# Kernel tuning notes

Measured on AMD Instinct MI355X. Metric: run time of the kernel, lower is better.

The kernel has to match this reference:

```python
import jax, jax.numpy as jnp
import numpy as np

D_HID = 512
N_HEADS = 16
D_HEAD = D_HID // N_HEADS  # 32
D_FFN = 2048
B, N = 4, 1024
FACTOR = 0.5 / np.sqrt(D_HEAD)
EPS = 1e-5


def layer_norm(x, g, b):
    m = x.mean(-1, keepdims=True)
    v = ((x - m) ** 2).mean(-1, keepdims=True)
    return (x - m) / jnp.sqrt(v + EPS) * g + b


def setup_inputs() -> dict:
    key = jax.random.key(0)
    ks = jax.random.split(key, 24)
    s = 0.02
    p = lambda k, shape: jax.random.normal(k, shape, jnp.float32) * s
    inp = {
        'H': jax.random.normal(ks[0], (B, N, D_HID), jnp.float32),
        'V': jax.random.normal(ks[1], (B, N, 3, D_HID), jnp.float32),
        'D_batch': jax.random.normal(ks[2], (B, N, N), jnp.float32),
        'rbf_bias': jax.random.normal(ks[3], (B, 1, N, N), jnp.float32),
        'H_mask': jax.random.randint(ks[4], (B, N), 0, 2, jnp.int32),
        # attention sublayer params
        'g1': jnp.ones((D_HID,), jnp.float32), 'beta1': jnp.zeros((D_HID,), jnp.float32),
        'Wq': p(ks[5], (D_HID, 4 * D_HID)), 'bq': p(ks[6], (4 * D_HID,)),
        'Wk': p(ks[7], (D_HID, 4 * D_HID)), 'bk': p(ks[8], (4 * D_HID,)),
        'Wv': p(ks[9], (D_HID, D_HID)), 'bv': p(ks[10], (D_HID,)),
        'Wvv': p(ks[11], (D_HID, D_HID)),
        'Wo': p(ks[12], (D_HID, D_HID)), 'bo': p(ks[13], (D_HID,)),
        'Wvo': p(ks[14], (D_HID, D_HID)),
        # GVP FFN sublayer params
        'g2': jnp.ones((D_HID,), jnp.float32), 'beta2': jnp.zeros((D_HID,), jnp.float32),
        'Wlv': p(ks[15], (D_HID, 2 * D_HID)),
        'W1': p(ks[16], (2 * D_HID, D_FFN)), 'b1f': p(ks[17], (D_FFN,)),
        'W2': p(ks[18], (D_FFN, 2 * D_HID)), 'b2f': p(ks[19], (2 * D_HID,)),
    }
    return inp


def ept_forward(H, V, D_batch, rbf_bias, H_mask, g1, beta1, Wq, bq, Wk, bk, Wv, bv,
                Wvv, Wo, bo, Wvo, g2, beta2, Wlv, W1, b1f, W2, b2f):
    b, n, d = H.shape
    # ---- attention sublayer (pre-LN on H only, residual on H and V) ----
    Hn = layer_norm(H, g1, beta1)
    Hq = (Hn @ Wq + bq).reshape(b, n, N_HEADS, 4 * D_HEAD)
    Hk = (Hn @ Wk + bk).reshape(b, n, N_HEADS, 4 * D_HEAD)
    Hv = (Hn @ Wv + bv).reshape(b, n, N_HEADS, D_HEAD)
    # vector values: [b,n,3,d] -> [b,n,heads,3*dh]
    Vv = (V @ Wvv).reshape(b, n, 3, N_HEADS, D_HEAD).transpose(0, 1, 3, 2, 4)
    Vv = Vv.reshape(b, n, N_HEADS, 3 * D_HEAD)
    V_attn = jnp.concatenate([Hv, Vv], axis=-1)  # [b,n,h,4*dh]
    bias = rbf_bias + D_batch[:, None]  # [b,1,n,n]
    keep = (H_mask != 0)[:, None, None, :]  # mask keys
    bias = jnp.where(keep, bias, -jnp.inf)
    logits = jnp.einsum('bnhd,bmhd->bhnm', Hq, Hk) * FACTOR + bias
    attn = jax.nn.softmax(logits, axis=-1)
    res = jnp.einsum('bhnm,bmhd->bnhd', attn, V_attn)  # [b,n,h,4*dh]
    H_res = res[..., :D_HEAD].reshape(b, n, d)
    V_res = res[..., D_HEAD:].reshape(b, n, N_HEADS, 3, D_HEAD)
    V_res = V_res.transpose(0, 1, 3, 2, 4).reshape(b, n, 3, d)
    H = H + H_res @ Wo + bo
    V = V + V_res @ Wvo
    # ---- GVP FFN sublayer (pre-LN on H only, residual) ----
    Hn2 = layer_norm(H, g2, beta2)
    Vp = V @ Wlv  # [b,n,3,2d]
    V1, V2 = Vp[..., :d], Vp[..., d:]
    scaler = jnp.concatenate([Hn2, jnp.sqrt((V1 ** 2).sum(axis=-2))], axis=-1)
    h = jax.nn.silu(scaler @ W1 + b1f) @ W2 + b2f  # [b,n,2d]
    H = H + h[..., :d]
    V = V + h[..., None, d:] * V2
    return H, V


def reference(H, V, D_batch, rbf_bias, H_mask, g1, beta1, Wq, bq, Wk, bk, Wv, bv,
              Wvv, Wo, bo, Wvo, g2, beta2, Wlv, W1, b1f, W2, b2f):
    return ept_forward(H, V, D_batch, rbf_bias, H_mask, g1, beta1, Wq, bq, Wk, bk,
                       Wv, bv, Wvv, Wo, bo, Wvo, g2, beta2, Wlv, W1, b1f, W2, b2f)
```

## Files before the change

### kernel.cpp

```cpp
#include <hip/hip_runtime.h>
#include <math.h>

#define NBATCH 4
#define NSEQ   1024
#define DHID   512
#define NHEADS 16
#define ROWS   (NBATCH*NSEQ)
#define VROWS  (ROWS*3)
#define ATT_FACTOR 0.08838834764831845f
#define LOG2E 1.4426950408889634f
#define F2 (ATT_FACTOR*LOG2E)
#define SM_SHIFT (16.0f*LOG2E)

typedef __attribute__((ext_vector_type(8))) short short8;
typedef __attribute__((ext_vector_type(4))) float floatx4;

#define AS1 __attribute__((address_space(1)))
#define AS3 __attribute__((address_space(3)))
#define GLOAD_LDS16(g, l) \
  __builtin_amdgcn_global_load_lds((const AS1 void*)(g), (AS3 void*)(l), 16, 0, 0)

__device__ __forceinline__ ushort f2bf(float x) {
  union { float f; unsigned u; } v; v.f = x;
  unsigned r = v.u + 0x7fff + ((v.u >> 16) & 1);
  return (ushort)(r >> 16);
}
__device__ __forceinline__ float bf2f(ushort u) {
  union { unsigned u; float f; } v; v.u = ((unsigned)u) << 16; return v.f;
}

template<int OBF>
__global__ __launch_bounds__(256) void ln_kernel(
    const float* __restrict__ x, void* __restrict__ y, int ystride,
    const float* __restrict__ g, const float* __restrict__ beta)
{
  int row = blockIdx.x;
  int t = threadIdx.x;
  const float* xr = x + (size_t)row * DHID;
  float2 v = ((const float2*)xr)[t];
  float s  = v.x + v.y;
  float ss = v.x*v.x + v.y*v.y;
  #pragma unroll
  for (int off = 32; off > 0; off >>= 1) {
    s  += __shfl_down(s, off);
    ss += __shfl_down(ss, off);
  }
  __shared__ float red[8];
  int w = t >> 6;
  if ((t & 63) == 0) { red[w*2] = s; red[w*2+1] = ss; }
  __syncthreads();
  s  = red[0] + red[2] + red[4] + red[6];
  ss = red[1] + red[3] + red[5] + red[7];
  float mean = s * (1.0f/DHID);
  float var  = ss * (1.0f/DHID) - mean*mean;
  float rstd = rsqrtf(var + 1e-5f);
  float2 gg = ((const float2*)g)[t];
  float2 bb = ((const float2*)beta)[t];
  float2 o;
  o.x = (v.x - mean) * rstd * gg.x + bb.x;
  o.y = (v.y - mean) * rstd * gg.y + bb.y;
  if constexpr (OBF) {
    ushort2 u = { f2bf(o.x), f2bf(o.y) };
    *(ushort2*)&((ushort*)y)[(size_t)row * ystride + 2*t] = u;
  } else {
    *(float2*)&((float*)y)[(size_t)row * ystride + 2*t] = o;
  }
}

struct WJobs {
  const float* src[9];
  ushort*      dst[9];
  int K[9];
  int N[9];
  int blk0[10];
};

__global__ __launch_bounds__(256) void wtrans_all_kernel(WJobs J)
{
  __shared__ float Ts[64][65];
  int bid = blockIdx.x;
  int j = 0;
  #pragma unroll
  for (int i = 1; i < 9; i++) if (bid >= J.blk0[i]) j = i;
  const float* W = J.src[j];
  ushort* Wt = J.dst[j];
  int K = J.K[j], N = J.N[j];
  int local = bid - J.blk0[j];
  int nx = N >> 6;
  int bx = local - (local / nx) * nx;
  int by = local / nx;
  int k0 = by*64, n0 = bx*64;
  int t = threadIdx.x;
  #pragma unroll
  for (int p = 0; p < 4; p++) {
    int f = p*256 + t;
    int r = f >> 4, c = (f & 15)*4;
    float4 v = *(const float4*)&W[(size_t)(k0+r)*N + n0 + c];
    Ts[r][c] = v.x; Ts[r][c+1] = v.y; Ts[r][c+2] = v.z; Ts[r][c+3] = v.w;
  }
  __syncthreads();
  #pragma unroll
  for (int p = 0; p < 2; p++) {
    int gidx = p*256 + t;
    int nr = gidx >> 3, kc = (gidx & 7)*8;
    ushort u[8];
    #pragma unroll
    for (int x = 0; x < 8; x++) u[x] = f2bf(Ts[kc+x][nr]);
    ushort4 a = {u[0],u[1],u[2],u[3]}, b4 = {u[4],u[5],u[6],u[7]};
    *(ushort4*)&Wt[(size_t)(n0+nr)*K + k0 + kc]     = a;
    *(ushort4*)&Wt[(size_t)(n0+nr)*K + k0 + kc + 4] = b4;
  }
}

__global__ __launch_bounds__(256) void conv_bf16_kernel(
    const float* __restrict__ x, ushort* __restrict__ y)
{
  int i = blockIdx.x*256 + threadIdx.x;
  float4 v = ((const float4*)x)[i];
  ushort4 u = { f2bf(v.x), f2bf(v.y), f2bf(v.z), f2bf(v.w) };
  ((ushort4*)y)[i] = u;
}

__global__ __launch_bounds__(256) void biascat_kernel(
    const float* __restrict__ bq, const float* __restrict__ bk,
    const float* __restrict__ bv, float* __restrict__ o)
{
  int i = blockIdx.x*256 + threadIdx.x;
  float v = (i < 2048) ? bq[i] : (i < 4096 ? bk[i-2048] : bv[i-4096]);
  o[i] = v;
}

template<int ACT, int HAS_BIAS, int HAS_RES, int OUT_BF16, int DUAL>
__global__ __launch_bounds__(256) void gemm_mfma_kernel(
    const ushort* __restrict__ A, const ushort* __restrict__ Bt,
    const float* __restrict__ bias, const float* __restrict__ resid,
    void* __restrict__ Cv, ushort* __restrict__ C2,
    int M, int N, int K)
{
  __shared__ ushort As[2][128*32];
  __shared__ ushort Bs[2][128*32];
  int t = threadIdx.x;
  int w = t >> 6, lane = t & 63;
  int q16 = lane & 15, quad = lane >> 4;
  int m0 = blockIdx.y * 128, n0 = blockIdx.x * 128;
  int wm = (w & 1) * 64, wn = (w >> 1) * 64;

  int r0 = t >> 2;
  int c0 = (t & 3) * 8;
  const ushort* Ag = A  + (size_t)(m0 + r0) * K + c0;
  const ushort* Bg = Bt + (size_t)(n0 + r0) * K + c0;
  int wb = w * 512;

  floatx4 acc[4][4];
  #pragma unroll
  for (int i = 0; i < 4; i++)
    #pragma unroll
    for (int j = 0; j < 4; j++) acc[i][j] = (floatx4){0.f,0.f,0.f,0.f};

  #define STAGE(buf, kk) do { \
    GLOAD_LDS16(Ag + (kk),                 &As[buf][wb]); \
    GLOAD_LDS16(Ag + (size_t)64*K + (kk),  &As[buf][2048 + wb]); \
    GLOAD_LDS16(Bg + (kk),                 &Bs[buf][wb]); \
    GLOAD_LDS16(Bg + (size_t)64*K + (kk),  &Bs[buf][2048 + wb]); \
  } while (0)

  STAGE(0, 0);
  __syncthreads();

  int nt = K >> 5;
  int cur = 0;
  for (int kt = 0; kt < nt; kt++) {
    if (kt + 1 < nt) STAGE(cur ^ 1, (kt + 1) * 32);
    short8 af[4], bf4[4];
    #pragma unroll
    for (int i = 0; i < 4; i++) {
      af[i]  = *(const short8*)&As[cur][(wm + i*16 + q16)*32 + quad*8];
      bf4[i] = *(const short8*)&Bs[cur][(wn + i*16 + q16)*32 + quad*8];
    }
    #pragma unroll
    for (int i = 0; i < 4; i++)
      #pragma unroll
      for (int j = 0; j < 4; j++)
        acc[i][j] = __builtin_amdgcn_mfma_f32_16x16x32_bf16(af[i], bf4[j], acc[i][j], 0, 0, 0);
    __syncthreads();
    cur ^= 1;
  }
  #undef STAGE

  float* Cf = (float*)Cv;
  ushort* Cu = (ushort*)Cv;
  float bj[4];
  #pragma unroll
  for (int j = 0; j < 4; j++)
    bj[j] = HAS_BIAS ? bias[n0 + wn + j*16 + q16] : 0.f;
  #pragma unroll
  for (int i = 0; i < 4; i++) {
    #pragma unroll
    for (int r = 0; r < 4; r++) {
      int row = m0 + wm + i*16 + quad*4 + r;
      size_t base = (size_t)row * N;
      #pragma unroll
      for (int j = 0; j < 4; j++) {
        int col = n0 + wn + j*16 + q16;
        float v = acc[i][j][r] + bj[j];
        if constexpr (ACT == 1) v = v / (1.f + __expf(-v));
        if constexpr (HAS_RES) v += resid[base + col];
        if constexpr (OUT_BF16) Cu[base + col] = f2bf(v);
        else                    Cf[base + col] = v;
        if constexpr (DUAL) C2[base + col] = f2bf(v);
      }
    }
  }
}

__global__ __launch_bounds__(256) void bias2_kernel(
    const float* __restrict__ Db, const float* __restrict__ Rb,
    const int* __restrict__ Mask, ushort* __restrict__ Bc2)
{
  int i2 = blockIdx.x*256 + threadIdx.x;
  int e = i2 * 2;
  int b = e >> 20;
  int m = e & 1023;
  float2 d = *(const float2*)&Db[e];
  float2 r = *(const float2*)&Rb[e];
  ushort2 o;
  o.x = Mask[b*NSEQ + m]     ? f2bf((d.x + r.x)*LOG2E) : f2bf(-1e30f);
  o.y = Mask[b*NSEQ + m + 1] ? f2bf((d.y + r.y)*LOG2E) : f2bf(-1e30f);
  *(ushort2*)&Bc2[e] = o;
}

__global__ __launch_bounds__(256) void vtrans_kernel(
    const ushort* __restrict__ QKV, const ushort* __restrict__ VVr,
    ushort* __restrict__ Vt)
{
  __shared__ float Ts[64][33];
  int t = threadIdx.x;
  int bh = blockIdx.z;
  int b = bh >> 4, h = bh & 15;
  int dt = blockIdx.y;
  int nt = blockIdx.x;
  int d0 = dt*32, n0 = nt*64;
  #pragma unroll
  for (int i = 0; i < 2; i++) {
    int nl = (t >> 3) + i*32;
    int c4 = (t & 7)*4;
    const ushort* src;
    if (dt == 0) src = &QKV[(size_t)(b*NSEQ + n0 + nl)*4608 + 4096 + h*32 + c4];
    else { int c = dt - 1; src = &VVr[((size_t)(b*NSEQ + n0 + nl)*3 + c)*512 + h*32 + c4]; }
    ushort4 v = *(const ushort4*)src;
    Ts[nl][c4] = bf2f(v.x); Ts[nl][c4+1] = bf2f(v.y);
    Ts[nl][c4+2] = bf2f(v.z); Ts[nl][c4+3] = bf2f(v.w);
  }
  __syncthreads();
  int dl = t >> 3;
  int n8 = (t & 7)*8;
  ushort u[8];
  #pragma unroll
  for (int k = 0; k < 8; k++) u[k] = f2bf(Ts[n8+k][dl]);
  size_t ob = ((size_t)bh*128 + d0 + dl)*NSEQ + n0 + n8;
  ushort4 u0 = {u[0],u[1],u[2],u[3]}, u1 = {u[4],u[5],u[6],u[7]};
  *(ushort4*)&Vt[ob]     = u0;
  *(ushort4*)&Vt[ob + 4] = u1;
}

__global__ __launch_bounds__(256, 2) void attn_mfma_kernel(
    const ushort* __restrict__ QKV,
    const ushort* __restrict__ Vt, const ushort* __restrict__ Bc2,
    ushort* __restrict__ HRES, ushort* __restrict__ VRES)
{
  __shared__ union {
    ushort q[128][136];
    struct {
      ushort k[64][136];
      ushort v[128][72];
      ushort bias[128][72];
    } s;
  } S;
  __shared__ ushort Ps[4][32][72];

  int t = threadIdx.x;
  int w = t >> 6, lane = t & 63;
  int q16 = lane & 15, quad = lane >> 4;
  int h = blockIdx.x, qt = blockIdx.y, b = blockIdx.z;
  int q0 = qt * 128;

  float4 rk0, rk1, rk2, rk3;
  float4 rv0, rv1, rv2, rv3;
  float4 rb0, rb1, rb2, rb3;
  const size_t kbase = (size_t)(b*NSEQ)*4608 + 2048 + h*128 + (t&3)*8;
  const size_t vbase = ((size_t)(b*NHEADS + h)*128 + (t>>3))*NSEQ + (t&7)*8;
  const size_t bbase = (size_t)(b*NSEQ + q0 + (t>>3))*NSEQ + (t&7)*8;
  int kr = t >> 2;
  int kc = (t & 3)*8;
  int vr = t >> 3, vc = (t & 7)*8;

  #define LOADT(m0_) do { \
    const ushort* kp = &QKV[kbase + (size_t)((m0_) + kr)*4608]; \
    rk0 = *(const float4*)(kp +  0); \
    rk1 = *(const float4*)(kp + 32); \
    rk2 = *(const float4*)(kp + 64); \
    rk3 = *(const float4*)(kp + 96); \
    const ushort* vp = &Vt[vbase + (m0_)]; \
    rv0 = *(const float4*)(vp + (size_t) 0*NSEQ); \
    rv1 = *(const float4*)(vp + (size_t)32*NSEQ); \
    rv2 = *(const float4*)(vp + (size_t)64*NSEQ); \
    rv3 = *(const float4*)(vp + (size_t)96*NSEQ); \
    const ushort* bp2 = &Bc2[bbase + (m0_)]; \
    rb0 = *(const float4*)(bp2 + (size_t) 0*NSEQ); \
    rb1 = *(const float4*)(bp2 + (size_t)32*NSEQ); \
    rb2 = *(const float4*)(bp2 + (size_t)64*NSEQ); \
    rb3 = *(const float4*)(bp2 + (size_t)96*NSEQ); \
  } while (0)

  #define STORET() do { \
    *(float4*)&S.s.k[kr][kc +  0] = rk0; \
    *(float4*)&S.s.k[kr][kc + 32] = rk1; \
    *(float4*)&S.s.k[kr][kc + 64] = rk2; \
    *(float4*)&S.s.k[kr][kc + 96] = rk3; \
    *(float4*)&S.s.v[vr +  0][vc] = rv0; \
    *(float4*)&S.s.v[vr + 32][vc] = rv1; \
    *(float4*)&S.s.v[vr + 64][vc] = rv2; \
    *(float4*)&S.s.v[vr + 96][vc] = rv3; \
    *(float4*)&S.s.bias[vr +  0][vc] = rb0; \
    *(float4*)&S.s.bias[vr + 32][vc] = rb1; \
    *(float4*)&S.s.bias[vr + 64][vc] = rb2; \
    *(float4*)&S.s.bias[vr + 96][vc] = rb3; \
  } while (0)

  LOADT(0);

  #pragma unroll
  for (int i = 0; i < 8; i++) {
    int f = t + i*256;
    int r = f >> 4, c8 = f & 15;
    *(float4*)&S.q[r][c8*8] =
        *(const float4*)&QKV[(size_t)(b*NSEQ + q0 + r)*4608 + h*128 + c8*8];
  }
  __syncthreads();
  short8 qf[2][4];
  #pragma unroll
  for (int rg = 0; rg < 2; rg++)
    #pragma unroll
    for (int c = 0; c < 4; c++)
      qf[rg][c] = *(const short8*)&S.q[w*32 + rg*16 + q16][c*32 + quad*8];

  floatx4 o[2][8];
  #pragma unroll
  for (int rg = 0; rg < 2; rg++)
    #pragma unroll
    for (int i = 0; i < 8; i++) o[rg][i] = (floatx4){0.f,0.f,0.f,0.f};
  float l_i[2][4] = {{0.f,0.f,0.f,0.f},{0.f,0.f,0.f,0.f}};

  #pragma unroll 1
  for (int it = 0; it < 16; it++) {
    __syncthreads();
    STORET();
    if (it < 15) LOADT((it + 1) * 64);
    __syncthreads();

    floatx4 sf[2][4];
    #pragma unroll
    for (int rg = 0; rg < 2; rg++)
      #pragma unroll
      for (int g = 0; g < 4; g++) sf[rg][g] = (floatx4){0.f,0.f,0.f,0.f};
    __builtin_amdgcn_s_setprio(1);
    #pragma unroll
    for (int c = 0; c < 4; c++) {
      short8 kf[4];
      #pragma unroll
      for (int g = 0; g < 4; g++)
        kf[g] = *(const short8*)&S.s.k[g*16 + q16][c*32 + quad*8];
      #pragma unroll
      for (int rg = 0; rg < 2; rg++)
        #pragma unroll
        for (int g = 0; g < 4; g++)
          sf[rg][g] = __builtin_amdgcn_mfma_f32_16x16x32_bf16(qf[rg][c], kf[g], sf[rg][g], 0, 0, 0);
    }
    __builtin_amdgcn_s_setprio(0);

    #pragma unroll
    for (int rg = 0; rg < 2; rg++) {
      #pragma unroll
      for (int i = 0; i < 4; i++) {
        int row = w*32 + rg*16 + quad*4 + i;
        #pragma unroll
        for (int g = 0; g < 4; g++) {
          float v = sf[rg][g][i]*F2 + bf2f(S.s.bias[row][g*16 + q16]);
          float p = exp2f(v - SM_SHIFT);
          Ps[w][rg*16 + quad*4 + i][g*16 + q16] = f2bf(p);
          l_i[rg][i] += p;
        }
      }
    }

    short8 pf[2][2];
    #pragma unroll
    for (int rg = 0; rg < 2; rg++)
      #pragma unroll
      for (int ks = 0; ks < 2; ks++)
        pf[rg][ks] = *(const short8*)&Ps[w][rg*16 + q16][ks*32 + quad*8];
    __builtin_amdgcn_s_setprio(1);
    #pragma unroll
    for (int tt = 0; tt < 8; tt++) {
      short8 vf0 = *(const short8*)&S.s.v[tt*16 + q16][quad*8];
      short8 vf1 = *(const short8*)&S.s.v[tt*16 + q16][32 + quad*8];
      #pragma unroll
      for (int rg = 0; rg < 2; rg++) {
        o[rg][tt] = __builtin_amdgcn_mfma_f32_16x16x32_bf16(pf[rg][0], vf0, o[rg][tt], 0, 0, 0);
        o[rg][tt] = __builtin_amdgcn_mfma_f32_16x16x32_bf16(pf[rg][1], vf1, o[rg][tt], 0, 0, 0);
      }
    }
    __builtin_amdgcn_s_setprio(0);
  }
  #undef LOADT
  #undef STORET

  #pragma unroll
  for (int rg = 0; rg < 2; rg++) {
    #pragma unroll
    for (int i = 0; i < 4; i++) {
      float l = l_i[rg][i];
      l += __shfl_xor(l, 1); l += __shfl_xor(l, 2);
      l += __shfl_xor(l, 4); l += __shfl_xor(l, 8);
      float inv = 1.0f / l;
      int grow = b*NSEQ + q0 + w*32 + rg*16 + quad*4 + i;
      #pragma unroll
      for (int tt = 0; tt < 2; tt++)
        HRES[(size_t)grow*512 + h*32 + tt*16 + q16] = f2bf(o[rg][tt][i] * inv);
      #pragma unroll
      for (int tt = 2; tt < 8; tt++) {
        int c = (tt - 2) >> 1;
        int jj = ((tt - 2) & 1)*16 + q16;
        VRES[((size_t)grow*3 + c)*512 + h*32 + jj] = f2bf(o[rg][tt][i] * inv);
      }
    }
  }
}

__global__ __launch_bounds__(256) void vnorm_kernel(
    const float* __restrict__ VP, ushort* __restrict__ SC)
{
  int idx = blockIdx.x*256 + threadIdx.x;
  int row = idx >> 9;
  int d = idx & 511;
  const float* p = VP + (size_t)row*3072 + d;
  float a = p[0], b = p[1024], c = p[2048];
  SC[(size_t)row*1024 + 512 + d] = f2bf(sqrtf(a*a + b*b + c*c));
}

__global__ __launch_bounds__(256) void finale_kernel(
    const float* __restrict__ HH, const float* __restrict__ VP,
    float* __restrict__ Hout, float* __restrict__ Vout)
{
  int idx = blockIdx.x*256 + threadIdx.x;
  if (idx < ROWS*DHID) {
    int row = idx >> 9;
    int d = idx & 511;
    Hout[idx] += HH[(size_t)row*1024 + d];
  } else {
    int k = idx - ROWS*DHID;
    int r3 = k >> 9;
    int d = k & 511;
    int row = r3 / 3;
    Vout[k] += HH[(size_t)row*1024 + 512 + d] * VP[(size_t)r3*1024 + 512 + d];
  }
}

extern "C" void kernel_launch(void* const* d_in, const int* in_sizes, int n_in,
                              void* d_out, int out_size, void* d_ws, size_t ws_size,
                              hipStream_t stream)
{
  const float* H    = (const float*)d_in[0];
  const float* V    = (const float*)d_in[1];
  const float* Db   = (const float*)d_in[2];
  const float* Rb   = (const float*)d_in[3];
  const int*   Mask = (const int*)d_in[4];
  const float* g1   = (const float*)d_in[5];
  const float* be1  = (const float*)d_in[6];
  const float* Wq   = (const float*)d_in[7];
  const float* bq   = (const float*)d_in[8];
  const float* Wk   = (const float*)d_in[9];
  const float* bkk  = (const float*)d_in[10];
  const float* Wv   = (const float*)d_in[11];
  const float* bv   = (const float*)d_in[12];
  const float* Wvv  = (const float*)d_in[13];
  const float* Wo   = (const float*)d_in[14];
  const float* bo   = (const float*)d_in[15];
  const float* Wvo  = (const float*)d_in[16];
  const float* g2   = (const float*)d_in[17];
  const float* be2  = (const float*)d_in[18];
  const float* Wlv  = (const float*)d_in[19];
  const float* W1   = (const float*)d_in[20];
  const float* b1f  = (const float*)d_in[21];
  const float* W2   = (const float*)d_in[22];
  const float* b2f  = (const float*)d_in[23];

  float* Hout = (float*)d_out;
  float* Vout = Hout + (size_t)ROWS*DHID;

  char* w = (char*)d_ws;
  const size_t MB = 1024*1024;
  const size_t KB = 1024;
  ushort* WqT  = (ushort*)(w + 0);
  ushort* WkT  = (ushort*)(w + 2048*KB);
  ushort* WvT  = (ushort*)(w + 4096*KB);
  ushort* WvvT = (ushort*)(w + 4608*KB);
  ushort* WoT  = (ushort*)(w + 5120*KB);
  ushort* WvoT = (ushort*)(w + 5632*KB);
  ushort* WlvT = (ushort*)(w + 6144*KB);
  ushort* W1T  = (ushort*)(w + 7168*KB);
  ushort* W2T  = (ushort*)(w + 11264*KB);
  float*  Bqkv = (float*)(w + 15360*KB);
  ushort* HNbf  = (ushort*)(w + 16*MB);
  ushort* QKVbf = (ushort*)(w + 20*MB);
  ushort* VVrbf = (ushort*)(w + 56*MB);
  ushort* Vbf   = (ushort*)(w + 68*MB);
  ushort* Vtb   = (ushort*)(w + 80*MB);
  ushort* Bc2   = (ushort*)(w + 96*MB);
  ushort* HRESbf = (ushort*)(w + 104*MB);
  ushort* VRESbf = (ushort*)(w + 108*MB);
  ushort* Voutbf = (ushort*)(w + 20*MB);
  float*  VP     = (float*)(w + 56*MB);
  ushort* SCbf   = (ushort*)(w + 104*MB);
  ushort* S1bf   = (ushort*)(w + 112*MB);
  float*  HHb    = (float*)(w + 32*MB);

  dim3 blk(256);

  WJobs J;
  const float* ws_[9] = {Wq, Wk, Wv, Wvv, Wo, Wvo, Wlv, W1, W2};
  ushort* wd_[9] = {WqT, WkT, WvT, WvvT, WoT, WvoT, WlvT, W1T, W2T};
  int wk_[9] = {512, 512, 512, 512, 512, 512, 512, 1024, 2048};
  int wn_[9] = {2048, 2048, 512, 512, 512, 512, 1024, 2048, 1024};
  int off = 0;
  for (int i = 0; i < 9; i++) {
    J.src[i] = ws_[i]; J.dst[i] = wd_[i]; J.K[i] = wk_[i]; J.N[i] = wn_[i];
    J.blk0[i] = off;
    off += (wn_[i] >> 6) * (wk_[i] >> 6);
  }
  J.blk0[9] = off;
  wtrans_all_kernel<<<off, blk, 0, stream>>>(J);

  ln_kernel<1><<<ROWS, blk, 0, stream>>>(H, HNbf, DHID, g1, be1);
  conv_bf16_kernel<<<(VROWS*DHID/4)/256, blk, 0, stream>>>(V, Vbf);
  biascat_kernel<<<18, blk, 0, stream>>>(bq, bkk, bv, Bqkv);

  gemm_mfma_kernel<0,1,0,1,0><<<dim3(36, 32), blk, 0, stream>>>(HNbf, WqT, Bqkv, nullptr, QKVbf, nullptr, 4096, 4608, 512);
  gemm_mfma_kernel<0,0,0,1,0><<<dim3( 4, 96), blk, 0, stream>>>(Vbf, WvvT, nullptr, nullptr, VVrbf, nullptr, 12288, 512, 512);

  bias2_kernel<<<(NBATCH*NSEQ*NSEQ/2)/256, blk, 0, stream>>>(Db, Rb, Mask, Bc2);
  vtrans_kernel<<<dim3(16, 4, 64), blk, 0, stream>>>(QKVbf, VVrbf, Vtb);

  attn_mfma_kernel<<<dim3(16, 8, 4), blk, 0, stream>>>(QKVbf, Vtb, Bc2, HRESbf, VRESbf);

  gemm_mfma_kernel<0,1,1,0,0><<<dim3(4, 32), blk, 0, stream>>>(HRESbf, WoT,  bo, H, Hout, nullptr, 4096, 512, 512);
  gemm_mfma_kernel<0,0,1,0,1><<<dim3(4, 96), blk, 0, stream>>>(VRESbf, WvoT, nullptr, V, Vout, Voutbf, 12288, 512, 512);

  ln_kernel<1><<<ROWS, blk, 0, stream>>>(Hout, SCbf, 1024, g2, be2);
  gemm_mfma_kernel<0,0,0,0,0><<<dim3(8, 96), blk, 0, stream>>>(Voutbf, WlvT, nullptr, nullptr, VP, nullptr, 12288, 1024, 512);
  vnorm_kernel<<<(ROWS*DHID)/256, blk, 0, stream>>>(VP, SCbf);

  gemm_mfma_kernel<1,1,0,1,0><<<dim3(16, 32), blk, 0, stream>>>(SCbf, W1T, b1f, nullptr, S1bf, nullptr, 4096, 2048, 1024);
  gemm_mfma_kernel<0,1,0,0,0><<<dim3( 8, 32), blk, 0, stream>>>(S1bf, W2T, b2f, nullptr, HHb, nullptr, 4096, 1024, 2048);

  finale_kernel<<<((ROWS + VROWS)*DHID)/256, blk, 0, stream>>>(HHb, VP, Hout, Vout);
}
```

Before: 480.3 us.

## Fuse Wo/Wvo output GEMMs and transpose score MFMA for vectorized softmax

```diff
diff --git a/kernel.cpp b/kernel.cpp
--- a/kernel.cpp
+++ b/kernel.cpp
@@ -213,6 +213,93 @@
   }
 }
 
+__global__ __launch_bounds__(256) void gemm_wovo_kernel(
+    const ushort* __restrict__ A,
+    const ushort* __restrict__ WoTp, const ushort* __restrict__ WvoTp,
+    const float* __restrict__ bo,
+    const float* __restrict__ Hres, const float* __restrict__ Vres,
+    float* __restrict__ Hout, float* __restrict__ Vout,
+    ushort* __restrict__ Voutbf)
+{
+  const int N = 512, K = 512;
+  __shared__ ushort As[2][128*32];
+  __shared__ ushort Bs[2][128*32];
+  int t = threadIdx.x;
+  int w = t >> 6, lane = t & 63;
+  int q16 = lane & 15, quad = lane >> 4;
+  int m0 = blockIdx.y * 128, n0 = blockIdx.x * 128;
+  int wm = (w & 1) * 64, wn = (w >> 1) * 64;
+  bool inH = (m0 < 4096);
+  const ushort* Bt = inH ? WoTp : WvoTp;
+
+  int r0 = t >> 2;
+  int c0 = (t & 3) * 8;
+  const ushort* Ag = A  + (size_t)(m0 + r0) * K + c0;
+  const ushort* Bg = Bt + (size_t)(n0 + r0) * K + c0;
+  int wb = w * 512;
+
+  floatx4 acc[4][4];
+  #pragma unroll
+  for (int i = 0; i < 4; i++)
+    #pragma unroll
+    for (int j = 0; j < 4; j++) acc[i][j] = (floatx4){0.f,0.f,0.f,0.f};
+
+  #define STAGE(buf, kk) do { \
+    GLOAD_LDS16(Ag + (kk),                 &As[buf][wb]); \
+    GLOAD_LDS16(Ag + (size_t)64*K + (kk),  &As[buf][2048 + wb]); \
+    GLOAD_LDS16(Bg + (kk),                 &Bs[buf][wb]); \
+    GLOAD_LDS16(Bg + (size_t)64*K + (kk),  &Bs[buf][2048 + wb]); \
+  } while (0)
+
+  STAGE(0, 0);
+  __syncthreads();
+
+  int cur = 0;
+  for (int kt = 0; kt < 16; kt++) {
+    if (kt + 1 < 16) STAGE(cur ^ 1, (kt + 1) * 32);
+    short8 af[4], bf4[4];
+    #pragma unroll
+    for (int i = 0; i < 4; i++) {
+      af[i]  = *(const short8*)&As[cur][(wm + i*16 + q16)*32 + quad*8];
+      bf4[i] = *(const short8*)&Bs[cur][(wn + i*16 + q16)*32 + quad*8];
+    }
+    #pragma unroll
+    for (int i = 0; i < 4; i++)
+      #pragma unroll
+      for (int j = 0; j < 4; j++)
+        acc[i][j] = __builtin_amdgcn_mfma_f32_16x16x32_bf16(af[i], bf4[j], acc[i][j], 0, 0, 0);
+    __syncthreads();
+    cur ^= 1;
+  }
+  #undef STAGE
+
+  float bj[4];
+  #pragma unroll
+  for (int j = 0; j < 4; j++)
+    bj[j] = inH ? bo[n0 + wn + j*16 + q16] : 0.f;
+  #pragma unroll
+  for (int i = 0; i < 4; i++) {
+    #pragma unroll
+    for (int r = 0; r < 4; r++) {
+      int row = m0 + wm + i*16 + quad*4 + r;
+      #pragma unroll
+      for (int j = 0; j < 4; j++) {
+        int col = n0 + wn + j*16 + q16;
+        float v = acc[i][j][r] + bj[j];
+        if (inH) {
+          size_t idx = (size_t)row * 512 + col;
+          Hout[idx] = v + Hres[idx];
+        } else {
+          size_t idx = (size_t)(row - 4096) * 512 + col;
+          float vv = v + Vres[idx];
+          Vout[idx] = vv;
+          Voutbf[idx] = f2bf(vv);
+        }
+      }
+    }
+  }
+}
+
 __global__ __launch_bounds__(256) void bias2_kernel(
     const float* __restrict__ Db, const float* __restrict__ Rb,
     const int* __restrict__ Mask, ushort* __restrict__ Bc2)
@@ -349,7 +436,7 @@
   for (int rg = 0; rg < 2; rg++)
     #pragma unroll
     for (int i = 0; i < 8; i++) o[rg][i] = (floatx4){0.f,0.f,0.f,0.f};
-  float l_i[2][4] = {{0.f,0.f,0.f,0.f},{0.f,0.f,0.f,0.f}};
+  float l_i[2] = {0.f, 0.f};
 
   #pragma unroll 1
   for (int it = 0; it < 16; it++) {
@@ -374,22 +461,26 @@
       for (int rg = 0; rg < 2; rg++)
         #pragma unroll
         for (int g = 0; g < 4; g++)
-          sf[rg][g] = __builtin_amdgcn_mfma_f32_16x16x32_bf16(qf[rg][c], kf[g], sf[rg][g], 0, 0, 0);
+          sf[rg][g] = __builtin_amdgcn_mfma_f32_16x16x32_bf16(kf[g], qf[rg][c], sf[rg][g], 0, 0, 0);
     }
     __builtin_amdgcn_s_setprio(0);
 
     #pragma unroll
     for (int rg = 0; rg < 2; rg++) {
-      #pragma unroll
-      for (int i = 0; i < 4; i++) {
-        int row = w*32 + rg*16 + quad*4 + i;
-        #pragma unroll
-        for (int g = 0; g < 4; g++) {
-          float v = sf[rg][g][i]*F2 + bf2f(S.s.bias[row][g*16 + q16]);
-          float p = exp2f(v - SM_SHIFT);
-          Ps[w][rg*16 + quad*4 + i][g*16 + q16] = f2bf(p);
-          l_i[rg][i] += p;
-        }
+      int brow = w*32 + rg*16 + q16;
+      #pragma unroll
+      for (int g = 0; g < 4; g++) {
+        ushort4 bb = *(const ushort4*)&S.s.bias[brow][g*16 + quad*4];
+        float p0 = exp2f(sf[rg][g][0]*F2 + bf2f(bb.x) - SM_SHIFT);
+        float p1 = exp2f(sf[rg][g][1]*F2 + bf2f(bb.y) - SM_SHIFT);
+        float p2 = exp2f(sf[rg][g][2]*F2 + bf2f(bb.z) - SM_SHIFT);
+        float p3 = exp2f(sf[rg][g][3]*F2 + bf2f(bb.w) - SM_SHIFT);
+        l_i[rg] += (p0 + p1) + (p2 + p3);
+        unsigned d0, d1;
+        asm("v_cvt_pk_bf16_f32 %0, %1, %2" : "=v"(d0) : "v"(p0), "v"(p1));
+        asm("v_cvt_pk_bf16_f32 %0, %1, %2" : "=v"(d1) : "v"(p2), "v"(p3));
+        uint2 dd = { d0, d1 };
+        *(uint2*)&Ps[w][rg*16 + q16][g*16 + quad*4] = dd;
       }
     }
 
@@ -417,12 +508,13 @@
 
   #pragma unroll
   for (int rg = 0; rg < 2; rg++) {
+    float l = l_i[rg];
+    l += __shfl_xor(l, 16);
+    l += __shfl_xor(l, 32);
     #pragma unroll
     for (int i = 0; i < 4; i++) {
-      float l = l_i[rg][i];
-      l += __shfl_xor(l, 1); l += __shfl_xor(l, 2);
-      l += __shfl_xor(l, 4); l += __shfl_xor(l, 8);
-      float inv = 1.0f / l;
+      float li = __shfl(l, quad*4 + i);
+      float inv = 1.0f / li;
       int grow = b*NSEQ + q0 + w*32 + rg*16 + quad*4 + i;
       #pragma unroll
       for (int tt = 0; tt < 2; tt++)
@@ -553,8 +645,7 @@
 
   attn_mfma_kernel<<<dim3(16, 8, 4), blk, 0, stream>>>(QKVbf, Vtb, Bc2, HRESbf, VRESbf);
 
-  gemm_mfma_kernel<0,1,1,0,0><<<dim3(4, 32), blk, 0, stream>>>(HRESbf, WoT,  bo, H, Hout, nullptr, 4096, 512, 512);
-  gemm_mfma_kernel<0,0,1,0,1><<<dim3(4, 96), blk, 0, stream>>>(VRESbf, WvoT, nullptr, V, Vout, Voutbf, 12288, 512, 512);
+  gemm_wovo_kernel<<<dim3(4, 128), blk, 0, stream>>>(HRESbf, WoT, WvoT, bo, H, V, Hout, Vout, Voutbf);
 
   ln_kernel<1><<<ROWS, blk, 0, stream>>>(Hout, SCbf, 1024, g2, be2);
   gemm_mfma_kernel<0,0,0,0,0><<<dim3(8, 96), blk, 0, stream>>>(Voutbf, WlvT, nullptr, nullptr, VP, nullptr, 12288, 1024, 512);
```

New measurement: 468.8 us. 1.02x faster.
